# Optimization experiments

Measured on AMD Instinct MI355X. Metric: run time of the kernel, lower is better.

Reference implementation:

```python
import jax, jax.numpy as jnp
import numpy as np

HIDDEN = 1024
NUM_QUBITS = 16
QUBIT_DIM = 64  # HIDDEN == NUM_QUBITS * QUBIT_DIM
LN_EPS = 1e-6   # flax nn.LayerNorm default


def setup_inputs() -> dict:
    key = jax.random.key(0)
    k_x, k_w = jax.random.split(key)
    B, S = 4, 4096
    x = jax.random.normal(k_x, (B, S, HIDDEN), dtype=jnp.float32)
    # Learned params (flax defaults: LN scale=ones, bias=zeros; Dense lecun_normal kernel, zero bias)
    ln_scale = jnp.ones((HIDDEN,), dtype=jnp.float32)
    ln_bias = jnp.zeros((HIDDEN,), dtype=jnp.float32)
    dense_w = jax.random.normal(k_w, (HIDDEN, HIDDEN), dtype=jnp.float32) * (1.0 / np.sqrt(HIDDEN))
    dense_b = jnp.zeros((HIDDEN,), dtype=jnp.float32)
    return {"x": x, "ln_scale": ln_scale, "ln_bias": ln_bias,
            "dense_w": dense_w, "dense_b": dense_b}


def reference(x, ln_scale, ln_bias, dense_w, dense_b):
    B, S, H = x.shape
    # input_preparation: LayerNorm over last axis, then reshape (B,S,Q,D)
    mean = jnp.mean(x, axis=-1, keepdims=True)
    var = jnp.mean(jnp.square(x - mean), axis=-1, keepdims=True)
    h = (x - mean) * jax.lax.rsqrt(var + LN_EPS) * ln_scale + ln_bias
    h = h.reshape(B, S, NUM_QUBITS, QUBIT_DIM)
    # quantum_forward (default jax backend): sin*cos, FFT along qubit axis, real part
    h = jnp.sin(h) * jnp.cos(h)
    h = jnp.real(jnp.fft.fft(h.astype(jnp.complex64), axis=-2))
    # post_process: restore (B,S,H) then Dense(hidden_size)
    h = h.reshape(B, S, H)
    return jnp.einsum('bsh,hk->bsk', h, dense_w) + dense_b
```

## Files before the change

### kernel.cpp

```cpp
#include <hip/hip_runtime.h>
#include <hip/hip_bf16.h>

#define HID 1024
#define MROWS 16384

typedef __bf16 bf16;
typedef __bf16 bf16x8 __attribute__((ext_vector_type(8)));
typedef float f32x4 __attribute__((ext_vector_type(4)));

#define MFMA(va, vb, vc) __builtin_amdgcn_mfma_f32_16x16x32_bf16(va, vb, vc, 0, 0, 0)

__global__ __launch_bounds__(256) void prepwt_k(const float* __restrict__ x,
                                                const float* __restrict__ gamma,
                                                const float* __restrict__ beta,
                                                const float* __restrict__ W,
                                                bf16* __restrict__ A,
                                                bf16* __restrict__ Wt) {
    const int bid = blockIdx.x;
    const int t = threadIdx.x;

    if (bid < 256) {
        const int idx = bid * 256 + t;
        const int n = idx >> 6;
        const int d = idx & 63;

        float wv[16];
#pragma unroll
        for (int qp = 0; qp < 16; ++qp)
            wv[qp] = W[(size_t)(qp * 64 + d) * HID + n];

        const float ct[16] = {
            1.0f,  0.92387953f,  0.70710678f,  0.38268343f,
            0.0f, -0.38268343f, -0.70710678f, -0.92387953f,
           -1.0f, -0.92387953f, -0.70710678f, -0.38268343f,
            0.0f,  0.38268343f,  0.70710678f,  0.92387953f};

#pragma unroll
        for (int q = 0; q < 16; ++q) {
            float acc = 0.0f;
#pragma unroll
            for (int qp = 0; qp < 16; ++qp) acc += wv[qp] * ct[(q * qp) & 15];
            Wt[(size_t)n * HID + q * 64 + d] = (bf16)acc;
        }
        return;
    }

    const int p = bid - 256;
    const int w = t >> 6, ln = t & 63;
    const int c0 = ln * 8;

    float4 ga0 = *(const float4*)&gamma[c0];
    float4 ga1 = *(const float4*)&gamma[c0 + 4];
    float4 ga2 = *(const float4*)&gamma[512 + c0];
    float4 ga3 = *(const float4*)&gamma[512 + c0 + 4];
    float4 be0 = *(const float4*)&beta[c0];
    float4 be1 = *(const float4*)&beta[c0 + 4];
    float4 be2 = *(const float4*)&beta[512 + c0];
    float4 be3 = *(const float4*)&beta[512 + c0 + 4];

#pragma unroll
    for (int rr = 0; rr < 2; ++rr) {
        const int row = p * 8 + rr * 4 + w;
        const float* xr = x + (size_t)row * HID;

        float4 v0 = *(const float4*)&xr[c0];
        float4 v1 = *(const float4*)&xr[c0 + 4];
        float4 v2 = *(const float4*)&xr[512 + c0];
        float4 v3 = *(const float4*)&xr[512 + c0 + 4];

        float s = v0.x + v0.y + v0.z + v0.w + v1.x + v1.y + v1.z + v1.w +
                  v2.x + v2.y + v2.z + v2.w + v3.x + v3.y + v3.z + v3.w;
        float ss = v0.x * v0.x + v0.y * v0.y + v0.z * v0.z + v0.w * v0.w +
                   v1.x * v1.x + v1.y * v1.y + v1.z * v1.z + v1.w * v1.w +
                   v2.x * v2.x + v2.y * v2.y + v2.z * v2.z + v2.w * v2.w +
                   v3.x * v3.x + v3.y * v3.y + v3.z * v3.z + v3.w * v3.w;
#pragma unroll
        for (int off = 32; off; off >>= 1) {
            s  += __shfl_xor(s, off);
            ss += __shfl_xor(ss, off);
        }
        const float mean = s * (1.0f / HID);
        const float rstd = rsqrtf(ss * (1.0f / HID) - mean * mean + 1e-6f);

        float h[16];
        h[0]  = (v0.x - mean) * rstd * ga0.x + be0.x;
        h[1]  = (v0.y - mean) * rstd * ga0.y + be0.y;
        h[2]  = (v0.z - mean) * rstd * ga0.z + be0.z;
        h[3]  = (v0.w - mean) * rstd * ga0.w + be0.w;
        h[4]  = (v1.x - mean) * rstd * ga1.x + be1.x;
        h[5]  = (v1.y - mean) * rstd * ga1.y + be1.y;
        h[6]  = (v1.z - mean) * rstd * ga1.z + be1.z;
        h[7]  = (v1.w - mean) * rstd * ga1.w + be1.w;
        h[8]  = (v2.x - mean) * rstd * ga2.x + be2.x;
        h[9]  = (v2.y - mean) * rstd * ga2.y + be2.y;
        h[10] = (v2.z - mean) * rstd * ga2.z + be2.z;
        h[11] = (v2.w - mean) * rstd * ga2.w + be2.w;
        h[12] = (v3.x - mean) * rstd * ga3.x + be3.x;
        h[13] = (v3.y - mean) * rstd * ga3.y + be3.y;
        h[14] = (v3.z - mean) * rstd * ga3.z + be3.z;
        h[15] = (v3.w - mean) * rstd * ga3.w + be3.w;

        bf16x8 o0, o1;
#pragma unroll
        for (int e = 0; e < 8; ++e) {
            o0[e] = (bf16)(0.5f * __sinf(2.0f * h[e]));
            o1[e] = (bf16)(0.5f * __sinf(2.0f * h[8 + e]));
        }
        *(bf16x8*)&A[(size_t)row * HID + c0] = o0;
        *(bf16x8*)&A[(size_t)row * HID + 512 + c0] = o1;
    }
}

#define BM 256
#define BN 256
#define BK 64
#define NT (HID / BK)

__global__ __launch_bounds__(512, 2) void gemm_k(const bf16* __restrict__ A,
                                                 const bf16* __restrict__ Bt,
                                                 const float* __restrict__ bias,
                                                 float* __restrict__ C) {
    __shared__ __attribute__((aligned(16))) char lds[131072];

    const int tid = threadIdx.x;
    const int w = tid >> 6, ln = tid & 63;
    const int wm = w >> 2, wn = w & 3;
    const int fr = ln & 15, fq = ln >> 4;

    int orig = blockIdx.x;
    int wg = (orig & 7) * 32 + (orig >> 3);
    int bm = wg >> 2, bn = wg & 3;

    const bf16* Ab = A + (size_t)bm * BM * HID;
    const bf16* Bb = Bt + (size_t)bn * BN * HID;

    auto stage = [&](int buf, int mat, int R0, int kt) {
        const char* gsrc = (const char*)(mat ? Bb : Ab);
        char* base = lds + (((buf << 1) | mat) << 15) + (R0 << 7);
        const int kb = kt << 7;
#pragma unroll
        for (int l = 0; l < 2; ++l) {
            int c = (l << 9) + tid;
            int lr = c >> 3;
            int colB = ((c & 7) ^ (lr & 7)) << 4;
            const char* g = gsrc + (size_t)(R0 + lr) * (HID * 2) + kb + colB;
            __builtin_amdgcn_global_load_lds(
                (const __attribute__((address_space(1))) void*)g,
                (__attribute__((address_space(3))) void*)(base + (((l << 9) + (w << 6)) << 4)),
                16, 0, 0);
        }
    };

    auto readA = [&](int buf, int i, int ks) -> bf16x8 {
        int r = ((i * 2 + wm) << 4) + fr;
        int off = (r << 7) + (ks << 6) + (fq << 4);
        off ^= (fr & 7) << 4;
        return *(const bf16x8*)(lds + ((buf << 1) << 15) + off);
    };
    auto readB = [&](int buf, int j, int ks) -> bf16x8 {
        int r = ((j * 4 + wn) << 4) + fr;
        int off = (r << 7) + (ks << 6) + (fq << 4);
        off ^= (fr & 7) << 4;
        return *(const bf16x8*)(lds + (((buf << 1) | 1) << 15) + off);
    };

    f32x4 acc[8][4];
#pragma unroll
    for (int i = 0; i < 8; ++i)
#pragma unroll
        for (int j = 0; j < 4; ++j) acc[i][j] = (f32x4){0.f, 0.f, 0.f, 0.f};

    stage(0, 1, 0, 0);
    stage(0, 0, 128, 0);
    stage(0, 0, 0, 0);
    stage(0, 1, 128, 0);
    stage(1, 1, 0, 1);
    stage(1, 0, 128, 1);
    asm volatile("s_waitcnt vmcnt(4)" ::: "memory");
    __builtin_amdgcn_s_barrier();

    bf16x8 a[8][2], b[4][2];

#pragma unroll 1
    for (int t = 0; t < NT; ++t) {
        const int cur = t & 1, nxt = cur ^ 1;

#pragma unroll
        for (int i = 0; i < 4; ++i) { a[i][0] = readA(cur, i, 0); a[i][1] = readA(cur, i, 1); }
#pragma unroll
        for (int j = 0; j < 2; ++j) { b[j][0] = readB(cur, j, 0); b[j][1] = readB(cur, j, 1); }
        if (t + 1 < NT) stage(nxt, 0, 0, t + 1);
        __builtin_amdgcn_s_barrier();
        asm volatile("s_waitcnt lgkmcnt(0)" ::: "memory");
        __builtin_amdgcn_sched_barrier(0);
        __builtin_amdgcn_s_setprio(1);
#pragma unroll
        for (int i = 0; i < 4; ++i)
#pragma unroll
            for (int j = 0; j < 2; ++j) {
                acc[i][j] = MFMA(a[i][0], b[j][0], acc[i][j]);
                acc[i][j] = MFMA(a[i][1], b[j][1], acc[i][j]);
            }
        __builtin_amdgcn_s_setprio(0);
        __builtin_amdgcn_s_barrier();

#pragma unroll
        for (int i = 4; i < 8; ++i) { a[i][0] = readA(cur, i, 0); a[i][1] = readA(cur, i, 1); }
        if (t + 1 < NT) stage(nxt, 1, 128, t + 1);
        __builtin_amdgcn_s_barrier();
        asm volatile("s_waitcnt lgkmcnt(0)" ::: "memory");
        __builtin_amdgcn_sched_barrier(0);
        __builtin_amdgcn_s_setprio(1);
#pragma unroll
        for (int i = 4; i < 8; ++i)
#pragma unroll
            for (int j = 0; j < 2; ++j) {
                acc[i][j] = MFMA(a[i][0], b[j][0], acc[i][j]);
                acc[i][j] = MFMA(a[i][1], b[j][1], acc[i][j]);
            }
        __builtin_amdgcn_s_setprio(0);
        __builtin_amdgcn_s_barrier();

#pragma unroll
        for (int j = 2; j < 4; ++j) { b[j][0] = readB(cur, j, 0); b[j][1] = readB(cur, j, 1); }
        if (t + 2 < NT) stage(cur, 1, 0, t + 2);
        __builtin_amdgcn_s_barrier();
        asm volatile("s_waitcnt lgkmcnt(0)" ::: "memory");
        __builtin_amdgcn_sched_barrier(0);
        __builtin_amdgcn_s_setprio(1);
#pragma unroll
        for (int i = 4; i < 8; ++i)
#pragma unroll
            for (int j = 2; j < 4; ++j) {
                acc[i][j] = MFMA(a[i][0], b[j][0], acc[i][j]);
                acc[i][j] = MFMA(a[i][1], b[j][1], acc[i][j]);
            }
        __builtin_amdgcn_s_setprio(0);
        __builtin_amdgcn_s_barrier();

        if (t + 2 < NT) stage(cur, 0, 128, t + 2);
        __builtin_amdgcn_s_barrier();
        __builtin_amdgcn_s_setprio(1);
#pragma unroll
        for (int i = 0; i < 4; ++i)
#pragma unroll
            for (int j = 2; j < 4; ++j) {
                acc[i][j] = MFMA(a[i][0], b[j][0], acc[i][j]);
                acc[i][j] = MFMA(a[i][1], b[j][1], acc[i][j]);
            }
        __builtin_amdgcn_s_setprio(0);
        if (t + 2 < NT) {
            asm volatile("s_waitcnt vmcnt(4)" ::: "memory");
        } else if (t + 1 < NT) {
            asm volatile("s_waitcnt vmcnt(0)" ::: "memory");
        }
        __builtin_amdgcn_sched_barrier(0);
        __builtin_amdgcn_s_barrier();
    }

#pragma unroll
    for (int j = 0; j < 4; ++j) {
        int col = bn * BN + ((j * 4 + wn) << 4) + fr;
        float bv = bias[col];
#pragma unroll
        for (int i = 0; i < 8; ++i) {
            int row0 = bm * BM + ((i * 2 + wm) << 4) + (fq << 2);
#pragma unroll
            for (int jj = 0; jj < 4; ++jj)
                C[(size_t)(row0 + jj) * HID + col] = acc[i][j][jj] + bv;
        }
    }
}

extern "C" void kernel_launch(void* const* d_in, const int* in_sizes, int n_in,
                              void* d_out, int out_size, void* d_ws, size_t ws_size,
                              hipStream_t stream) {
    const float* x   = (const float*)d_in[0];
    const float* lng = (const float*)d_in[1];
    const float* lnb = (const float*)d_in[2];
    const float* W   = (const float*)d_in[3];
    const float* db  = (const float*)d_in[4];
    float* out = (float*)d_out;

    bf16* A  = (bf16*)d_ws;
    bf16* Wt = (bf16*)((char*)d_ws + (size_t)MROWS * HID * 2);

    prepwt_k<<<256 + MROWS / 8, 256, 0, stream>>>(x, lng, lnb, W, A, Wt);
    gemm_k<<<(MROWS / BM) * (HID / BN), 512, 0, stream>>>(A, Wt, db, out);
}
```

Before: 66.69 us.

## Fuse LayerNorm apply and sin transform into GEMM A-tile staging

The first kernel now computes only per-row mean/rstd statistics plus the DFT-folded weight, and no longer writes the bf16 activation matrix. The GEMM loads fp32 x tiles into registers, applies normalization, gamma/beta and the sin transform, then writes bf16 directly into the LDS A buffer. This removes the write and re-read of the 32 MB bf16 intermediate. In exchange, x (fp32, twice the bytes) is re-read by each of the four column-block workgroups, the prefetch depth drops to one tile, and transcendental work now sits inside the MFMA loop.

Result: slower. 116.9 us (+75.3%).

```diff
diff --git a/kernel.cpp b/kernel.cpp
--- a/kernel.cpp
+++ b/kernel.cpp
@@ -10,12 +10,10 @@
 
 #define MFMA(va, vb, vc) __builtin_amdgcn_mfma_f32_16x16x32_bf16(va, vb, vc, 0, 0, 0)
 
-__global__ __launch_bounds__(256) void prepwt_k(const float* __restrict__ x,
-                                                const float* __restrict__ gamma,
-                                                const float* __restrict__ beta,
-                                                const float* __restrict__ W,
-                                                bf16* __restrict__ A,
-                                                bf16* __restrict__ Wt) {
+__global__ __launch_bounds__(256) void statswt_k(const float* __restrict__ x,
+                                                 const float* __restrict__ W,
+                                                 float2* __restrict__ stats,
+                                                 bf16* __restrict__ Wt) {
     const int bid = blockIdx.x;
     const int t = threadIdx.x;
 
@@ -48,15 +46,6 @@
     const int p = bid - 256;
     const int w = t >> 6, ln = t & 63;
     const int c0 = ln * 8;
-
-    float4 ga0 = *(const float4*)&gamma[c0];
-    float4 ga1 = *(const float4*)&gamma[c0 + 4];
-    float4 ga2 = *(const float4*)&gamma[512 + c0];
-    float4 ga3 = *(const float4*)&gamma[512 + c0 + 4];
-    float4 be0 = *(const float4*)&beta[c0];
-    float4 be1 = *(const float4*)&beta[c0 + 4];
-    float4 be2 = *(const float4*)&beta[512 + c0];
-    float4 be3 = *(const float4*)&beta[512 + c0 + 4];
 
 #pragma unroll
     for (int rr = 0; rr < 2; ++rr) {
@@ -81,33 +70,7 @@
         }
         const float mean = s * (1.0f / HID);
         const float rstd = rsqrtf(ss * (1.0f / HID) - mean * mean + 1e-6f);
-
-        float h[16];
-        h[0]  = (v0.x - mean) * rstd * ga0.x + be0.x;
-        h[1]  = (v0.y - mean) * rstd * ga0.y + be0.y;
-        h[2]  = (v0.z - mean) * rstd * ga0.z + be0.z;
-        h[3]  = (v0.w - mean) * rstd * ga0.w + be0.w;
-        h[4]  = (v1.x - mean) * rstd * ga1.x + be1.x;
-        h[5]  = (v1.y - mean) * rstd * ga1.y + be1.y;
-        h[6]  = (v1.z - mean) * rstd * ga1.z + be1.z;
-        h[7]  = (v1.w - mean) * rstd * ga1.w + be1.w;
-        h[8]  = (v2.x - mean) * rstd * ga2.x + be2.x;
-        h[9]  = (v2.y - mean) * rstd * ga2.y + be2.y;
-        h[10] = (v2.z - mean) * rstd * ga2.z + be2.z;
-        h[11] = (v2.w - mean) * rstd * ga2.w + be2.w;
-        h[12] = (v3.x - mean) * rstd * ga3.x + be3.x;
-        h[13] = (v3.y - mean) * rstd * ga3.y + be3.y;
-        h[14] = (v3.z - mean) * rstd * ga3.z + be3.z;
-        h[15] = (v3.w - mean) * rstd * ga3.w + be3.w;
-
-        bf16x8 o0, o1;
-#pragma unroll
-        for (int e = 0; e < 8; ++e) {
-            o0[e] = (bf16)(0.5f * __sinf(2.0f * h[e]));
-            o1[e] = (bf16)(0.5f * __sinf(2.0f * h[8 + e]));
-        }
-        *(bf16x8*)&A[(size_t)row * HID + c0] = o0;
-        *(bf16x8*)&A[(size_t)row * HID + 512 + c0] = o1;
+        if (ln == 0) stats[row] = make_float2(mean, rstd);
     }
 }
 
@@ -116,11 +79,17 @@
 #define BK 64
 #define NT (HID / BK)
 
-__global__ __launch_bounds__(512, 2) void gemm_k(const bf16* __restrict__ A,
+__global__ __launch_bounds__(512, 2) void gemm_k(const float* __restrict__ x,
+                                                 const float* __restrict__ gamma,
+                                                 const float* __restrict__ beta,
+                                                 const float2* __restrict__ stats,
                                                  const bf16* __restrict__ Bt,
                                                  const float* __restrict__ bias,
                                                  float* __restrict__ C) {
     __shared__ __attribute__((aligned(16))) char lds[131072];
+    __shared__ float2 sStats[256];
+    __shared__ __attribute__((aligned(16))) float sG[1024];
+    __shared__ __attribute__((aligned(16))) float sBe[1024];
 
     const int tid = threadIdx.x;
     const int w = tid >> 6, ln = tid & 63;
@@ -130,24 +99,67 @@
     int orig = blockIdx.x;
     int wg = (orig & 7) * 32 + (orig >> 3);
     int bm = wg >> 2, bn = wg & 3;
-
-    const bf16* Ab = A + (size_t)bm * BM * HID;
+    const int m0 = bm * BM;
+
     const bf16* Bb = Bt + (size_t)bn * BN * HID;
 
-    auto stage = [&](int buf, int mat, int R0, int kt) {
-        const char* gsrc = (const char*)(mat ? Bb : Ab);
-        char* base = lds + (((buf << 1) | mat) << 15) + (R0 << 7);
+    auto stageB = [&](int buf, int R0, int kt) {
+        char* base = lds + (((buf << 1) | 1) << 15) + (R0 << 7);
         const int kb = kt << 7;
 #pragma unroll
         for (int l = 0; l < 2; ++l) {
             int c = (l << 9) + tid;
             int lr = c >> 3;
             int colB = ((c & 7) ^ (lr & 7)) << 4;
-            const char* g = gsrc + (size_t)(R0 + lr) * (HID * 2) + kb + colB;
+            const char* g = (const char*)Bb + (size_t)(R0 + lr) * (HID * 2) + kb + colB;
             __builtin_amdgcn_global_load_lds(
                 (const __attribute__((address_space(1))) void*)g,
                 (__attribute__((address_space(3))) void*)(base + (((l << 9) + (w << 6)) << 4)),
                 16, 0, 0);
+        }
+    };
+
+    int Rf_[4], scu_[4];
+    size_t xoff_[4];
+#pragma unroll
+    for (int cc = 0; cc < 4; ++cc) {
+        int rl = ((cc & 1) << 6) + (tid >> 3);
+        int Rf = ((cc >> 1) << 7) + rl;
+        int scu = (tid & 7) ^ (rl & 7);
+        Rf_[cc] = Rf; scu_[cc] = scu;
+        xoff_[cc] = (size_t)(m0 + Rf) * HID + scu * 8;
+    }
+
+    auto loadx = [&](int kt, f32x4* xr) {
+#pragma unroll
+        for (int cc = 0; cc < 4; ++cc) {
+            const float* p = x + xoff_[cc] + kt * BK;
+            xr[cc * 2]     = *(const f32x4*)p;
+            xr[cc * 2 + 1] = *(const f32x4*)(p + 4);
+        }
+    };
+
+    auto xform = [&](int buf, int kt, f32x4* xr) {
+        char* Abase = lds + ((buf << 1) << 15);
+#pragma unroll
+        for (int cc = 0; cc < 4; ++cc) {
+            float2 st = sStats[Rf_[cc]];
+            const float mu = st.x, rs = st.y;
+            int gb = kt * BK + scu_[cc] * 8;
+            float4 g0 = *(const float4*)&sG[gb], g1 = *(const float4*)&sG[gb + 4];
+            float4 e0 = *(const float4*)&sBe[gb], e1 = *(const float4*)&sBe[gb + 4];
+            f32x4 lo = xr[cc * 2], hi = xr[cc * 2 + 1];
+            bf16x8 o;
+            o[0] = (bf16)(0.5f * __sinf(2.0f * ((lo[0] - mu) * rs * g0.x + e0.x)));
+            o[1] = (bf16)(0.5f * __sinf(2.0f * ((lo[1] - mu) * rs * g0.y + e0.y)));
+            o[2] = (bf16)(0.5f * __sinf(2.0f * ((lo[2] - mu) * rs * g0.z + e0.z)));
+            o[3] = (bf16)(0.5f * __sinf(2.0f * ((lo[3] - mu) * rs * g0.w + e0.w)));
+            o[4] = (bf16)(0.5f * __sinf(2.0f * ((hi[0] - mu) * rs * g1.x + e1.x)));
+            o[5] = (bf16)(0.5f * __sinf(2.0f * ((hi[1] - mu) * rs * g1.y + e1.y)));
+            o[6] = (bf16)(0.5f * __sinf(2.0f * ((hi[2] - mu) * rs * g1.z + e1.z)));
+            o[7] = (bf16)(0.5f * __sinf(2.0f * ((hi[3] - mu) * rs * g1.w + e1.w)));
+            char* d = Abase + ((cc >> 1) << 14) + ((((cc & 1) << 9) + tid) << 4);
+            *(bf16x8*)d = o;
         }
     };
 
@@ -170,13 +182,19 @@
 #pragma unroll
         for (int j = 0; j < 4; ++j) acc[i][j] = (f32x4){0.f, 0.f, 0.f, 0.f};
 
-    stage(0, 1, 0, 0);
-    stage(0, 0, 128, 0);
-    stage(0, 0, 0, 0);
-    stage(0, 1, 128, 0);
-    stage(1, 1, 0, 1);
-    stage(1, 0, 128, 1);
-    asm volatile("s_waitcnt vmcnt(4)" ::: "memory");
+    if (tid < 256) sStats[tid] = stats[m0 + tid];
+    sG[tid] = gamma[tid];  sG[tid + 512] = gamma[tid + 512];
+    sBe[tid] = beta[tid];  sBe[tid + 512] = beta[tid + 512];
+
+    f32x4 xr[8];
+    loadx(0, xr);
+    stageB(0, 0, 0);
+    stageB(0, 128, 0);
+    asm volatile("s_waitcnt lgkmcnt(0)" ::: "memory");
+    __builtin_amdgcn_s_barrier();
+    asm volatile("s_waitcnt vmcnt(0)" ::: "memory");
+    xform(0, 0, xr);
+    asm volatile("s_waitcnt lgkmcnt(0)" ::: "memory");
     __builtin_amdgcn_s_barrier();
 
     bf16x8 a[8][2], b[4][2];
@@ -189,7 +207,7 @@
         for (int i = 0; i < 4; ++i) { a[i][0] = readA(cur, i, 0); a[i][1] = readA(cur, i, 1); }
 #pragma unroll
         for (int j = 0; j < 2; ++j) { b[j][0] = readB(cur, j, 0); b[j][1] = readB(cur, j, 1); }
-        if (t + 1 < NT) stage(nxt, 0, 0, t + 1);
+        if (t + 1 < NT) loadx(t + 1, xr);
         __builtin_amdgcn_s_barrier();
         asm volatile("s_waitcnt lgkmcnt(0)" ::: "memory");
         __builtin_amdgcn_sched_barrier(0);
@@ -206,7 +224,7 @@
 
 #pragma unroll
         for (int i = 4; i < 8; ++i) { a[i][0] = readA(cur, i, 0); a[i][1] = readA(cur, i, 1); }
-        if (t + 1 < NT) stage(nxt, 1, 128, t + 1);
+        if (t + 1 < NT) stageB(nxt, 128, t + 1);
         __builtin_amdgcn_s_barrier();
         asm volatile("s_waitcnt lgkmcnt(0)" ::: "memory");
         __builtin_amdgcn_sched_barrier(0);
@@ -223,7 +241,7 @@
 
 #pragma unroll
         for (int j = 2; j < 4; ++j) { b[j][0] = readB(cur, j, 0); b[j][1] = readB(cur, j, 1); }
-        if (t + 2 < NT) stage(cur, 1, 0, t + 2);
+        if (t + 1 < NT) stageB(nxt, 0, t + 1);
         __builtin_amdgcn_s_barrier();
         asm volatile("s_waitcnt lgkmcnt(0)" ::: "memory");
         __builtin_amdgcn_sched_barrier(0);
@@ -238,8 +256,6 @@
         __builtin_amdgcn_s_setprio(0);
         __builtin_amdgcn_s_barrier();
 
-        if (t + 2 < NT) stage(cur, 0, 128, t + 2);
-        __builtin_amdgcn_s_barrier();
         __builtin_amdgcn_s_setprio(1);
 #pragma unroll
         for (int i = 0; i < 4; ++i)
@@ -249,10 +265,11 @@
                 acc[i][j] = MFMA(a[i][1], b[j][1], acc[i][j]);
             }
         __builtin_amdgcn_s_setprio(0);
-        if (t + 2 < NT) {
-            asm volatile("s_waitcnt vmcnt(4)" ::: "memory");
-        } else if (t + 1 < NT) {
+        if (t + 1 < NT) {
             asm volatile("s_waitcnt vmcnt(0)" ::: "memory");
+            __builtin_amdgcn_sched_barrier(0);
+            xform(nxt, t + 1, xr);
+            asm volatile("s_waitcnt lgkmcnt(0)" ::: "memory");
         }
         __builtin_amdgcn_sched_barrier(0);
         __builtin_amdgcn_s_barrier();
@@ -282,9 +299,9 @@
     const float* db  = (const float*)d_in[4];
     float* out = (float*)d_out;
 
-    bf16* A  = (bf16*)d_ws;
-    bf16* Wt = (bf16*)((char*)d_ws + (size_t)MROWS * HID * 2);
-
-    prepwt_k<<<256 + MROWS / 8, 256, 0, stream>>>(x, lng, lnb, W, A, Wt);
-    gemm_k<<<(MROWS / BM) * (HID / BN), 512, 0, stream>>>(A, Wt, db, out);
+    float2* stats = (float2*)d_ws;
+    bf16* Wt = (bf16*)((char*)d_ws + (size_t)MROWS * 8);
+
+    statswt_k<<<256 + MROWS / 8, 256, 0, stream>>>(x, W, stats, Wt);
+    gemm_k<<<(MROWS / BM) * (HID / BN), 512, 0, stream>>>(x, lng, lnb, stats, Wt, db, out);
 }
```
